# Kernel optimization log

Hardware: AMD Instinct MI355X
Metric: run time of the kernel (lower is better)

## Reference

```python
import jax, jax.numpy as jnp
import numpy as np

D_MODEL = 1024
N_HEADS = 16
N_GROUPS = 4
D_HEAD = D_MODEL // N_HEADS  # 64
HPG = N_HEADS // N_GROUPS    # heads per KV group = 4
B, T = 2, 2048


def _rope(x):
    # x: [B, H, T, D]; interleaved even/odd rotary, matching the torch module
    t, d = x.shape[2], x.shape[3]
    pos = jnp.arange(t, dtype=jnp.float32)[:, None]                      # [T,1]
    freq = jnp.exp(-(jnp.arange(0, d, 2, dtype=jnp.float32) / d)
                   * jnp.log(jnp.float32(10000.0)))                      # [D/2]
    angle = pos * freq                                                   # [T, D/2]
    cos, sin = jnp.cos(angle), jnp.sin(angle)
    xe, xo = x[..., ::2], x[..., 1::2]
    re = xe * cos - xo * sin
    ro = xe * sin + xo * cos
    return jnp.stack([re, ro], axis=-1).reshape(x.shape)


def setup_inputs() -> dict:
    key = jax.random.key(0)
    ks = jax.random.split(key, 10)
    s = 0.02
    return {
        "x":  jax.random.normal(ks[0], (B, T, D_MODEL), dtype=jnp.float32),
        "Wq": jax.random.normal(ks[1], (D_MODEL, D_MODEL), dtype=jnp.float32) * s,
        "bq": jax.random.normal(ks[2], (D_MODEL,), dtype=jnp.float32) * s,
        "Wk": jax.random.normal(ks[3], (D_MODEL, N_GROUPS * D_HEAD), dtype=jnp.float32) * s,
        "bk": jax.random.normal(ks[4], (N_GROUPS * D_HEAD,), dtype=jnp.float32) * s,
        "Wv": jax.random.normal(ks[5], (D_MODEL, N_GROUPS * D_HEAD), dtype=jnp.float32) * s,
        "bv": jax.random.normal(ks[6], (N_GROUPS * D_HEAD,), dtype=jnp.float32) * s,
        "Wo": jax.random.normal(ks[7], (D_MODEL, D_MODEL), dtype=jnp.float32) * s,
        "bo": jax.random.normal(ks[8], (D_MODEL,), dtype=jnp.float32) * s,
    }


def reference(x, Wq, bq, Wk, bk, Wv, bv, Wo, bo):
    b, t, _ = x.shape
    q = (x @ Wq + bq).reshape(b, t, N_HEADS, D_HEAD).transpose(0, 2, 1, 3)    # [B,H,T,D]
    k = (x @ Wk + bk).reshape(b, t, N_GROUPS, D_HEAD).transpose(0, 2, 1, 3)   # [B,G,T,D]
    v = (x @ Wv + bv).reshape(b, t, N_GROUPS, D_HEAD).transpose(0, 2, 1, 3)
    # GQA broadcast: idx = arange(n_heads) // heads_per_group  ==  repeat each group HPG times
    k = jnp.repeat(k, HPG, axis=1)                                            # [B,H,T,D]
    v = jnp.repeat(v, HPG, axis=1)
    q = _rope(q)
    k = _rope(k)
    scale = jnp.float32(np.sqrt(D_HEAD))
    scores = jnp.einsum('bhtd,bhsd->bhts', q, k) / scale                      # [B,H,T,T]
    causal = jnp.tril(jnp.ones((t, t), dtype=bool))
    scores = jnp.where(causal, scores, -jnp.inf)
    probs = jax.nn.softmax(scores, axis=-1)
    # dropout(p=0.05) is identity in eval mode
    attn = jnp.einsum('bhts,bhsd->bhtd', probs, v)
    out = attn.transpose(0, 2, 1, 3).reshape(b, t, N_HEADS * D_HEAD)
    return out @ Wo + bo
```

## Files before the change

kernel.cpp:

```cpp
#include <hip/hip_runtime.h>
#include <stdint.h>

typedef unsigned short u16;
typedef __attribute__((ext_vector_type(4))) float f32x4;
typedef __attribute__((ext_vector_type(8))) short bf16x8;
typedef __attribute__((ext_vector_type(4))) short bf16x4;

#define T_SEQ 2048
#define DM 1024
#define NH 16
#define NG 4
#define DH 64
#define QSCALE 0.18033688011112042f

__device__ __forceinline__ u16 f2bf(float f) {
    union { float f; uint32_t u; } v; v.f = f;
    uint32_t r = (v.u + 0x7FFFu + ((v.u >> 16) & 1u)) >> 16;
    return (u16)r;
}
__device__ __forceinline__ float bf2f(u16 u) {
    union { uint32_t u; float f; } v; v.u = ((uint32_t)u) << 16;
    return v.f;
}
__device__ __forceinline__ float fexp2(float x) {
#if __has_builtin(__builtin_amdgcn_exp2f)
    return __builtin_amdgcn_exp2f(x);
#else
    return exp2f(x);
#endif
}
__device__ __forceinline__ uint32_t cvtpk_bf16(float a, float b) {
    uint32_t r;
    asm("v_cvt_pk_bf16_f32 %0, %1, %2" : "=v"(r) : "v"(a), "v"(b));
    return r;
}

#if __has_builtin(__builtin_amdgcn_mfma_f32_16x16x16_bf16)
__device__ __forceinline__ f32x4 mfma16(bf16x4 a, bf16x4 b, f32x4 c) {
    return __builtin_amdgcn_mfma_f32_16x16x16_bf16(a, b, c, 0, 0, 0);
}
#elif __has_builtin(__builtin_amdgcn_mfma_f32_16x16x16bf16_1k)
__device__ __forceinline__ f32x4 mfma16(bf16x4 a, bf16x4 b, f32x4 c) {
    return __builtin_amdgcn_mfma_f32_16x16x16bf16_1k(a, b, c, 0, 0, 0);
}
#else
__device__ __forceinline__ f32x4 mfma16(bf16x4 a, bf16x4 b, f32x4 c) {
    asm("v_mfma_f32_16x16x16_bf16 %0, %1, %2, %0" : "+v"(c) : "v"(a), "v"(b));
    return c;
}
#endif

__device__ __forceinline__ void async16(const void* g, void* l) {
    __builtin_amdgcn_global_load_lds(
        (const __attribute__((address_space(1))) void*)g,
        (__attribute__((address_space(3))) void*)l,
        16, 0, 0);
}

__global__ __launch_bounds__(256) void k_prep(
    const float* __restrict__ x, u16* __restrict__ xb,
    const float* __restrict__ Wq, const float* __restrict__ Wk,
    const float* __restrict__ Wv, const float* __restrict__ Wo,
    u16* __restrict__ wqkvt, u16* __restrict__ wot,
    const float* __restrict__ bq, const float* __restrict__ bk,
    const float* __restrict__ bv, float* __restrict__ bqkv,
    float2* __restrict__ tbl) {
    int blk = blockIdx.x;
    int tid = threadIdx.x;
    if (blk < 2048) {
        int i = blk * 256 + tid;
        const float4* p = (const float4*)x + (size_t)i * 2;
        float4 a = p[0], b = p[1];
        bf16x8 v;
        v[0] = (short)f2bf(a.x); v[1] = (short)f2bf(a.y);
        v[2] = (short)f2bf(a.z); v[3] = (short)f2bf(a.w);
        v[4] = (short)f2bf(b.x); v[5] = (short)f2bf(b.y);
        v[6] = (short)f2bf(b.z); v[7] = (short)f2bf(b.w);
        ((bf16x8*)xb)[i] = v;
        return;
    }
    int t = blk - 2048;
    if (t >= 2560) {
        int u = t - 2560;
        if (u < 6) {
            int i = u * 256 + tid;
            if (i < 1536) {
                float v;
                if (i < 1024) v = bq[i];
                else if (i < 1280) v = bk[i - 1024];
                else v = bv[i - 1280];
                bqkv[i] = v;
            }
        } else {
            int idx = (u - 6) * 256 + tid;
            int tt = idx >> 5, i = idx & 31;
            float freq = exp2f(-(float)i * (13.287712379549449f / 32.0f));
            float ang = (float)tt * freq;
            tbl[idx] = make_float2(cosf(ang), sinf(ang));
        }
        return;
    }
    const float* src; u16* dst; int N;
    if (t < 1024)      { src = Wq; dst = wqkvt;                      N = 1024; }
    else if (t < 1280) { t -= 1024; src = Wk; dst = wqkvt + (size_t)1024 * 1024; N = 256; }
    else if (t < 1536) { t -= 1280; src = Wv; dst = wqkvt + (size_t)1280 * 1024; N = 256; }
    else               { t -= 1536; src = Wo; dst = wot;             N = 1024; }
    int ntiles = N >> 5;
    int n0 = (t % ntiles) * 32, k0 = (t / ntiles) * 32;
    __shared__ float tile[32][33];
    int tx = tid & 31, ty = tid >> 5;
#pragma unroll
    for (int q = 0; q < 4; q++)
        tile[ty + q * 8][tx] = src[(size_t)(k0 + ty + q * 8) * N + n0 + tx];
    __syncthreads();
#pragma unroll
    for (int q = 0; q < 4; q++)
        dst[(size_t)(n0 + ty + q * 8) * 1024 + k0 + tx] = f2bf(tile[tx][ty + q * 8]);
}

template <int EPI>
__global__ __launch_bounds__(256) void k_gemm(
    const u16* __restrict__ A, const u16* __restrict__ Bt,
    const float* __restrict__ bias, float* __restrict__ C,
    const float2* __restrict__ tbl, u16* __restrict__ Qo,
    u16* __restrict__ Ko, u16* __restrict__ Vto, int N, int K) {
    __shared__ __align__(16) u16 As[2][64 * 64];
    __shared__ __align__(16) u16 Bs[2][128 * 64];
    int tid = threadIdx.x;
    int lane = tid & 63, wid = tid >> 6;
    int wr = wid >> 1, wc = wid & 1;
    int l15 = lane & 15, lhi = lane >> 4;
    int row0 = blockIdx.y * 64, col0 = blockIdx.x * 128;
    f32x4 acc[2][4] = {};

    const u16* ga[2];
    const u16* gb[4];
#pragma unroll
    for (int i = 0; i < 2; i++) {
        int c = i * 256 + tid, r = c >> 3, sch = (c & 7) ^ (r & 7);
        ga[i] = A + (size_t)(row0 + r) * K + sch * 8;
    }
#pragma unroll
    for (int i = 0; i < 4; i++) {
        int c = i * 256 + tid, r = c >> 3, sch = (c & 7) ^ (r & 7);
        gb[i] = Bt + (size_t)(col0 + r) * K + sch * 8;
    }

#pragma unroll
    for (int i = 0; i < 2; i++) async16(ga[i], &As[0][(i * 256 + tid) * 8]);
#pragma unroll
    for (int i = 0; i < 4; i++) async16(gb[i], &Bs[0][(i * 256 + tid) * 8]);
    __syncthreads();

    int nk = K >> 6;
    for (int kt = 0; kt < nk; kt++) {
        int cur = kt & 1;
        if (kt + 1 < nk) {
            int nx = cur ^ 1, ko = (kt + 1) << 6;
#pragma unroll
            for (int i = 0; i < 2; i++) async16(ga[i] + ko, &As[nx][(i * 256 + tid) * 8]);
#pragma unroll
            for (int i = 0; i < 4; i++) async16(gb[i] + ko, &Bs[nx][(i * 256 + tid) * 8]);
        }
        const u16* Ac = As[cur];
        const u16* Bc = Bs[cur];
#pragma unroll
        for (int ks = 0; ks < 2; ks++) {
            bf16x8 af[2], bfr[4];
#pragma unroll
            for (int m = 0; m < 2; m++) {
                int r = wr * 32 + m * 16 + l15;
                int kb = (ks * 64 + lhi * 16) ^ ((r & 7) << 4);
                af[m] = *(const bf16x8*)((const char*)Ac + r * 128 + kb);
            }
#pragma unroll
            for (int n = 0; n < 4; n++) {
                int r = wc * 64 + n * 16 + l15;
                int kb = (ks * 64 + lhi * 16) ^ ((r & 7) << 4);
                bfr[n] = *(const bf16x8*)((const char*)Bc + r * 128 + kb);
            }
#pragma unroll
            for (int m = 0; m < 2; m++)
#pragma unroll
                for (int n = 0; n < 4; n++)
                    acc[m][n] = __builtin_amdgcn_mfma_f32_16x16x32_bf16(
                        af[m], bfr[n], acc[m][n], 0, 0, 0);
        }
        __syncthreads();
    }

    if (EPI == 0) {
#pragma unroll
        for (int n = 0; n < 4; n++) {
            int col = col0 + wc * 64 + n * 16 + l15;
            float bv = bias[col];
#pragma unroll
            for (int m = 0; m < 2; m++) {
                int row = row0 + wr * 32 + m * 16 + lhi * 4;
#pragma unroll
                for (int i = 0; i < 4; i++)
                    C[(size_t)(row + i) * N + col] = acc[m][n][i] + bv;
            }
        }
    } else {
        int type = (col0 >= 1280) ? 2 : (col0 >= 1024 ? 1 : 0);
        int rbase = row0 + wr * 32;
#pragma unroll
        for (int n = 0; n < 4; n++) {
            int col = col0 + wc * 64 + n * 16 + l15;
            float bv = bias[col];
            if (type == 2) {
                int cc = col - 1280;
                int g = cc >> 6, d = cc & 63;
#pragma unroll
                for (int m = 0; m < 2; m++)
#pragma unroll
                    for (int i = 0; i < 4; i++) {
                        int rowg = rbase + m * 16 + lhi * 4 + i;
                        int t = rowg & (T_SEQ - 1), b = rowg >> 11;
                        int sp = t ^ ((d & 1) << 2);
                        Vto[(((size_t)(b * NG + g)) * DH + d) * T_SEQ + sp] =
                            f2bf(acc[m][n][i] + bv);
                    }
            } else {
                float ssgn = (col & 1) ? 1.f : -1.f;
                int ip = (col & 63) >> 1;
#pragma unroll
                for (int m = 0; m < 2; m++)
#pragma unroll
                    for (int i = 0; i < 4; i++) {
                        int rowg = rbase + m * 16 + lhi * 4 + i;
                        int t = rowg & (T_SEQ - 1), b = rowg >> 11;
                        float v = acc[m][n][i] + bv;
                        float other = __shfl_xor(v, 1);
                        float2 cs = tbl[t * 32 + ip];
                        float out = v * cs.x + other * cs.y * ssgn;
                        if (type == 0) {
                            int h = col >> 6, d = col & 63;
                            Qo[(((size_t)(b * NH + h)) * T_SEQ + t) * DH + d] =
                                f2bf(out * QSCALE);
                        } else {
                            int cc = col - 1024;
                            int g = cc >> 6, d = cc & 63;
                            Ko[(((size_t)(b * NG + g)) * T_SEQ + t) * DH + d] = f2bf(out);
                        }
                    }
            }
        }
    }
}

__global__ __launch_bounds__(256) void k_attn(
    const u16* __restrict__ Q, const u16* __restrict__ K,
    const u16* __restrict__ Vt, u16* __restrict__ Aout) {
    int i0 = blockIdx.x;
    int u = i0 >> 5;
    int qt = (u < 16) ? (31 - u) : (u - 16);
    int bh = i0 & 31;
    int b = bh >> 4, h = bh & 15, g = h >> 2;
    int tid = threadIdx.x;
    int lane = tid & 63, wid = tid >> 6;
    int l15 = lane & 15, lhi = lane >> 4;

    const u16* Kp = K + ((size_t)(b * NG + g)) * T_SEQ * DH;
    const u16* Vp = Vt + ((size_t)(b * NG + g)) * DH * T_SEQ;

    __shared__ __align__(16) u16 Ks[2][64 * 64];
    __shared__ __align__(16) u16 Vs[3][64 * 64];

    const u16* Qp = Q + ((size_t)bh * T_SEQ + qt * 64) * DH;
    bf16x8 qf[2];
#pragma unroll
    for (int ks = 0; ks < 2; ks++)
        qf[ks] = *(const bf16x8*)(Qp + (size_t)(wid * 16 + l15) * DH + ks * 32 + lhi * 8);

    f32x4 of[4] = {};
    float l_i = 0.f;

    int nt = qt + 1;
    int swz = (l15 & 7) << 4;

    int c0 = tid, c1 = tid + 256;
    int rk0 = c0 >> 3, rk1 = c1 >> 3;
    int sk0 = (c0 & 7) ^ (rk0 & 7);
    int sk1 = (c1 & 7) ^ (rk1 & 7);
    int sv0 = (c0 & 7) ^ ((rk0 >> 1) & 7);
    int sv1 = (c1 & 7) ^ ((rk1 >> 1) & 7);
    const u16* kg0 = Kp + rk0 * DH + sk0 * 8;
    const u16* kg1 = Kp + rk1 * DH + sk1 * 8;
    const u16* vg0 = Vp + (size_t)rk0 * T_SEQ + sv0 * 8;
    const u16* vg1 = Vp + (size_t)rk1 * T_SEQ + sv1 * 8;

    async16(kg0, &Ks[0][c0 * 8]);
    async16(kg1, &Ks[0][c1 * 8]);
    async16(vg0, &Vs[0][c0 * 8]);
    async16(vg1, &Vs[0][c1 * 8]);
    __syncthreads();
    if (nt > 1) {
        async16(kg0 + (1 << 12), &Ks[1][c0 * 8]);
        async16(kg1 + (1 << 12), &Ks[1][c1 * 8]);
        async16(vg0 + (1 << 6), &Vs[1][c0 * 8]);
        async16(vg1 + (1 << 6), &Vs[1][c1 * 8]);
    }
    f32x4 sf[4] = {};
    __builtin_amdgcn_s_setprio(1);
#pragma unroll
    for (int ks = 0; ks < 2; ks++)
#pragma unroll
        for (int n = 0; n < 4; n++) {
            int kb = (ks * 64 + lhi * 16) ^ swz;
            bf16x8 kf = *(const bf16x8*)((const char*)Ks[0] + (n * 16 + l15) * 128 + kb);
            sf[n] = __builtin_amdgcn_mfma_f32_16x16x32_bf16(kf, qf[ks], sf[n], 0, 0, 0);
        }
    __builtin_amdgcn_s_setprio(0);
    __syncthreads();

    u16* vread = Vs[0];
    u16* vhold = Vs[1];
    u16* vstage = Vs[2];

#pragma unroll 1
    for (int it = 1; it < nt; it++) {
        if (it + 1 < nt) {
            int ko = (it + 1) << 12, vo = (it + 1) << 6;
            int nx = (it + 1) & 1;
            async16(kg0 + ko, &Ks[nx][c0 * 8]);
            async16(kg1 + ko, &Ks[nx][c1 * 8]);
            async16(vg0 + vo, vstage + c0 * 8);
            async16(vg1 + vo, vstage + c1 * 8);
        }

        bf16x4 pa[4];
#pragma unroll
        for (int n = 0; n < 4; n++) {
            float p0 = fexp2(sf[n][0]);
            float p1 = fexp2(sf[n][1]);
            float p2 = fexp2(sf[n][2]);
            float p3 = fexp2(sf[n][3]);
            l_i += p0 + p1 + p2 + p3;
            union { uint32_t uu[2]; bf16x4 v; } pu;
            pu.uu[0] = cvtpk_bf16(p0, p1);
            pu.uu[1] = cvtpk_bf16(p2, p3);
            pa[n] = pu.v;
        }

        const u16* Kc = Ks[it & 1];
        __builtin_amdgcn_s_setprio(1);
#pragma unroll
        for (int ks = 0; ks < 2; ks++)
#pragma unroll
            for (int n = 0; n < 4; n++) {
                int kb = (ks * 64 + lhi * 16) ^ swz;
                bf16x8 kf = *(const bf16x8*)((const char*)Kc + (n * 16 + l15) * 128 + kb);
                f32x4 z = (ks == 0) ? f32x4{0.f, 0.f, 0.f, 0.f} : sf[n];
                sf[n] = __builtin_amdgcn_mfma_f32_16x16x32_bf16(kf, qf[ks], z, 0, 0, 0);
            }

#pragma unroll
        for (int nd = 0; nd < 4; nd++) {
            int rowb = (nd * 16 + l15) * 128;
#pragma unroll
            for (int n = 0; n < 4; n++) {
                int kb = ((4 * n + lhi) ^ l15) << 3;
                bf16x4 vf = *(const bf16x4*)((const char*)vread + rowb + kb);
                of[nd] = mfma16(pa[n], vf, of[nd]);
            }
        }
        __builtin_amdgcn_s_setprio(0);

        u16* tmp = vread; vread = vhold; vhold = vstage; vstage = tmp;
        __syncthreads();
    }

    {
        int qrow = qt * 64 + wid * 16 + l15;
        int sb = (nt - 1) * 64 + lhi * 4;
#pragma unroll
        for (int n = 0; n < 4; n++)
#pragma unroll
            for (int i = 0; i < 4; i++)
                if (sb + n * 16 + i > qrow) sf[n][i] = -3.0e38f;
        bf16x4 pa[4];
#pragma unroll
        for (int n = 0; n < 4; n++) {
            float p0 = fexp2(sf[n][0]);
            float p1 = fexp2(sf[n][1]);
            float p2 = fexp2(sf[n][2]);
            float p3 = fexp2(sf[n][3]);
            l_i += p0 + p1 + p2 + p3;
            union { uint32_t uu[2]; bf16x4 v; } pu;
            pu.uu[0] = cvtpk_bf16(p0, p1);
            pu.uu[1] = cvtpk_bf16(p2, p3);
            pa[n] = pu.v;
        }
        __builtin_amdgcn_s_setprio(1);
#pragma unroll
        for (int nd = 0; nd < 4; nd++) {
            int rowb = (nd * 16 + l15) * 128;
#pragma unroll
            for (int n = 0; n < 4; n++) {
                int kb = ((4 * n + lhi) ^ l15) << 3;
                bf16x4 vf = *(const bf16x4*)((const char*)vread + rowb + kb);
                of[nd] = mfma16(pa[n], vf, of[nd]);
            }
        }
        __builtin_amdgcn_s_setprio(0);
    }

#pragma unroll
    for (int off = 16; off <= 32; off <<= 1)
        l_i += __shfl_xor(l_i, off);
    float lq[4];
#pragma unroll
    for (int i = 0; i < 4; i++)
        lq[i] = __shfl(l_i, lhi * 4 + i);
#pragma unroll
    for (int n = 0; n < 4; n++)
#pragma unroll
        for (int i = 0; i < 4; i++) {
            int trow = qt * 64 + wid * 16 + lhi * 4 + i;
            float v = of[n][i] / lq[i];
            Aout[((size_t)(b * T_SEQ + trow)) * DM + h * 64 + n * 16 + l15] = f2bf(v);
        }
}

extern "C" void kernel_launch(void* const* d_in, const int* in_sizes, int n_in,
                              void* d_out, int out_size, void* d_ws, size_t ws_size,
                              hipStream_t stream) {
    const float* x  = (const float*)d_in[0];
    const float* Wq = (const float*)d_in[1];
    const float* bq = (const float*)d_in[2];
    const float* Wk = (const float*)d_in[3];
    const float* bk = (const float*)d_in[4];
    const float* Wv = (const float*)d_in[5];
    const float* bv = (const float*)d_in[6];
    const float* Wo = (const float*)d_in[7];
    const float* bo = (const float*)d_in[8];

    char* ws = (char*)d_ws;
    size_t o = 0;
    u16*   xb    = (u16*)(ws + o);  o += (size_t)4096 * 1024 * 2;
    u16*   wqkvt = (u16*)(ws + o);  o += (size_t)1536 * 1024 * 2;
    u16*   wot   = (u16*)(ws + o);  o += (size_t)1024 * 1024 * 2;
    float* bqkv  = (float*)(ws + o); o += 1536 * 4;
    o = (o + 255) & ~(size_t)255;
    u16*   Qb    = (u16*)(ws + o);  o += (size_t)2 * NH * T_SEQ * DH * 2;
    u16*   Kb    = (u16*)(ws + o);  o += (size_t)2 * NG * T_SEQ * DH * 2;
    u16*   Vtb   = (u16*)(ws + o);  o += (size_t)2 * NG * DH * T_SEQ * 2;
    u16*   attnb = (u16*)(ws + o);  o += (size_t)4096 * 1024 * 2;
    float2* tbl  = (float2*)(ws + o); o += (size_t)2048 * 32 * 8;

    k_prep<<<4870, 256, 0, stream>>>(x, xb, Wq, Wk, Wv, Wo, wqkvt, wot, bq, bk, bv, bqkv, tbl);
    k_gemm<1><<<dim3(12, 64), 256, 0, stream>>>(xb, wqkvt, bqkv, nullptr, tbl, Qb, Kb, Vtb, 1536, 1024);
    k_attn<<<1024, 256, 0, stream>>>(Qb, Kb, Vtb, attnb);
    k_gemm<0><<<dim3(8, 64), 256, 0, stream>>>(attnb, wot, bo, (float*)d_out, nullptr, nullptr, nullptr, nullptr, 1024, 1024);
}
```

Measured before the change: 87.37 us.

## Process two 64-row query tiles per attention block to reuse K/V tiles

Each attention workgroup now handles 128 query rows (two 64-row sub-tiles) instead of 64, so every K/V tile staged into shared memory feeds twice as many MFMAs. The grid is halved to 512 blocks and the causal masking is split across the two sub-tiles' diagonal steps. The aim is to cut global-to-LDS traffic and barrier overhead per unit of work. In exchange, register pressure roughly doubles for scores and accumulators, and there are fewer blocks to balance the causal workload across CUs.

```diff
diff --git a/kernel.cpp b/kernel.cpp
--- a/kernel.cpp
+++ b/kernel.cpp
@@ -255,7 +255,7 @@
     const u16* __restrict__ Vt, u16* __restrict__ Aout) {
     int i0 = blockIdx.x;
     int u = i0 >> 5;
-    int qt = (u < 16) ? (31 - u) : (u - 16);
+    int qt = (u < 8) ? (15 - u) : (u - 8);
     int bh = i0 & 31;
     int b = bh >> 4, h = bh & 15, g = h >> 2;
     int tid = threadIdx.x;
@@ -268,16 +268,19 @@
     __shared__ __align__(16) u16 Ks[2][64 * 64];
     __shared__ __align__(16) u16 Vs[3][64 * 64];
 
-    const u16* Qp = Q + ((size_t)bh * T_SEQ + qt * 64) * DH;
-    bf16x8 qf[2];
-#pragma unroll
-    for (int ks = 0; ks < 2; ks++)
-        qf[ks] = *(const bf16x8*)(Qp + (size_t)(wid * 16 + l15) * DH + ks * 32 + lhi * 8);
-
-    f32x4 of[4] = {};
-    float l_i = 0.f;
-
-    int nt = qt + 1;
+    const u16* Qp = Q + ((size_t)bh * T_SEQ + qt * 128) * DH;
+    bf16x8 qf[2][2];
+#pragma unroll
+    for (int qq = 0; qq < 2; qq++)
+#pragma unroll
+        for (int ks = 0; ks < 2; ks++)
+            qf[qq][ks] = *(const bf16x8*)(Qp + (size_t)(qq * 64 + wid * 16 + l15) * DH +
+                                          ks * 32 + lhi * 8);
+
+    f32x4 of[2][4] = {};
+    float l0 = 0.f, l1 = 0.f;
+
+    int nt = 2 * qt + 2;
     int swz = (l15 & 7) << 4;
 
     int c0 = tid, c1 = tid + 256;
@@ -296,13 +299,13 @@
     async16(vg0, &Vs[0][c0 * 8]);
     async16(vg1, &Vs[0][c1 * 8]);
     __syncthreads();
-    if (nt > 1) {
+    {
         async16(kg0 + (1 << 12), &Ks[1][c0 * 8]);
         async16(kg1 + (1 << 12), &Ks[1][c1 * 8]);
         async16(vg0 + (1 << 6), &Vs[1][c0 * 8]);
         async16(vg1 + (1 << 6), &Vs[1][c1 * 8]);
     }
-    f32x4 sf[4] = {};
+    f32x4 sf[2][4] = {};
     __builtin_amdgcn_s_setprio(1);
 #pragma unroll
     for (int ks = 0; ks < 2; ks++)
@@ -310,7 +313,8 @@
         for (int n = 0; n < 4; n++) {
             int kb = (ks * 64 + lhi * 16) ^ swz;
             bf16x8 kf = *(const bf16x8*)((const char*)Ks[0] + (n * 16 + l15) * 128 + kb);
-            sf[n] = __builtin_amdgcn_mfma_f32_16x16x32_bf16(kf, qf[ks], sf[n], 0, 0, 0);
+            sf[0][n] = __builtin_amdgcn_mfma_f32_16x16x32_bf16(kf, qf[0][ks], sf[0][n], 0, 0, 0);
+            sf[1][n] = __builtin_amdgcn_mfma_f32_16x16x32_bf16(kf, qf[1][ks], sf[1][n], 0, 0, 0);
         }
     __builtin_amdgcn_s_setprio(0);
     __syncthreads();
@@ -330,18 +334,33 @@
             async16(vg1 + vo, vstage + c1 * 8);
         }
 
-        bf16x4 pa[4];
+        if (it == nt - 1) {
+            int qrow = qt * 128 + wid * 16 + l15;
+            int sb = (nt - 2) * 64 + lhi * 4;
+#pragma unroll
+            for (int n = 0; n < 4; n++)
+#pragma unroll
+                for (int i = 0; i < 4; i++)
+                    if (sb + n * 16 + i > qrow) sf[0][n][i] = -3.0e38f;
+        }
+
+        bf16x4 pa[2][4];
 #pragma unroll
         for (int n = 0; n < 4; n++) {
-            float p0 = fexp2(sf[n][0]);
-            float p1 = fexp2(sf[n][1]);
-            float p2 = fexp2(sf[n][2]);
-            float p3 = fexp2(sf[n][3]);
-            l_i += p0 + p1 + p2 + p3;
+            float a0 = fexp2(sf[0][n][0]), a1 = fexp2(sf[0][n][1]);
+            float a2 = fexp2(sf[0][n][2]), a3 = fexp2(sf[0][n][3]);
+            l0 += a0 + a1 + a2 + a3;
             union { uint32_t uu[2]; bf16x4 v; } pu;
-            pu.uu[0] = cvtpk_bf16(p0, p1);
-            pu.uu[1] = cvtpk_bf16(p2, p3);
-            pa[n] = pu.v;
+            pu.uu[0] = cvtpk_bf16(a0, a1);
+            pu.uu[1] = cvtpk_bf16(a2, a3);
+            pa[0][n] = pu.v;
+            float b0 = fexp2(sf[1][n][0]), b1 = fexp2(sf[1][n][1]);
+            float b2 = fexp2(sf[1][n][2]), b3 = fexp2(sf[1][n][3]);
+            l1 += b0 + b1 + b2 + b3;
+            union { uint32_t uu[2]; bf16x4 v; } pv;
+            pv.uu[0] = cvtpk_bf16(b0, b1);
+            pv.uu[1] = cvtpk_bf16(b2, b3);
+            pa[1][n] = pv.v;
         }
 
         const u16* Kc = Ks[it & 1];
@@ -352,8 +371,10 @@
             for (int n = 0; n < 4; n++) {
                 int kb = (ks * 64 + lhi * 16) ^ swz;
                 bf16x8 kf = *(const bf16x8*)((const char*)Kc + (n * 16 + l15) * 128 + kb);
-                f32x4 z = (ks == 0) ? f32x4{0.f, 0.f, 0.f, 0.f} : sf[n];
-                sf[n] = __builtin_amdgcn_mfma_f32_16x16x32_bf16(kf, qf[ks], z, 0, 0, 0);
+                f32x4 z0 = (ks == 0) ? f32x4{0.f, 0.f, 0.f, 0.f} : sf[0][n];
+                f32x4 z1 = (ks == 0) ? f32x4{0.f, 0.f, 0.f, 0.f} : sf[1][n];
+                sf[0][n] = __builtin_amdgcn_mfma_f32_16x16x32_bf16(kf, qf[0][ks], z0, 0, 0, 0);
+                sf[1][n] = __builtin_amdgcn_mfma_f32_16x16x32_bf16(kf, qf[1][ks], z1, 0, 0, 0);
             }
 
 #pragma unroll
@@ -363,7 +384,8 @@
             for (int n = 0; n < 4; n++) {
                 int kb = ((4 * n + lhi) ^ l15) << 3;
                 bf16x4 vf = *(const bf16x4*)((const char*)vread + rowb + kb);
-                of[nd] = mfma16(pa[n], vf, of[nd]);
+                of[0][nd] = mfma16(pa[0][n], vf, of[0][nd]);
+                of[1][nd] = mfma16(pa[1][n], vf, of[1][nd]);
             }
         }
         __builtin_amdgcn_s_setprio(0);
@@ -373,25 +395,28 @@
     }
 
     {
-        int qrow = qt * 64 + wid * 16 + l15;
+#pragma unroll
+        for (int n = 0; n < 4; n++)
+#pragma unroll
+            for (int i = 0; i < 4; i++)
+                sf[0][n][i] = -3.0e38f;
+        int qrow = qt * 128 + 64 + wid * 16 + l15;
         int sb = (nt - 1) * 64 + lhi * 4;
 #pragma unroll
         for (int n = 0; n < 4; n++)
 #pragma unroll
             for (int i = 0; i < 4; i++)
-                if (sb + n * 16 + i > qrow) sf[n][i] = -3.0e38f;
-        bf16x4 pa[4];
+                if (sb + n * 16 + i > qrow) sf[1][n][i] = -3.0e38f;
+        bf16x4 pa[2][4];
 #pragma unroll
         for (int n = 0; n < 4; n++) {
-            float p0 = fexp2(sf[n][0]);
-            float p1 = fexp2(sf[n][1]);
-            float p2 = fexp2(sf[n][2]);
-            float p3 = fexp2(sf[n][3]);
-            l_i += p0 + p1 + p2 + p3;
-            union { uint32_t uu[2]; bf16x4 v; } pu;
-            pu.uu[0] = cvtpk_bf16(p0, p1);
-            pu.uu[1] = cvtpk_bf16(p2, p3);
-            pa[n] = pu.v;
+            float b0 = fexp2(sf[1][n][0]), b1 = fexp2(sf[1][n][1]);
+            float b2 = fexp2(sf[1][n][2]), b3 = fexp2(sf[1][n][3]);
+            l1 += b0 + b1 + b2 + b3;
+            union { uint32_t uu[2]; bf16x4 v; } pv;
+            pv.uu[0] = cvtpk_bf16(b0, b1);
+            pv.uu[1] = cvtpk_bf16(b2, b3);
+            pa[1][n] = pv.v;
         }
         __builtin_amdgcn_s_setprio(1);
 #pragma unroll
@@ -401,27 +426,34 @@
             for (int n = 0; n < 4; n++) {
                 int kb = ((4 * n + lhi) ^ l15) << 3;
                 bf16x4 vf = *(const bf16x4*)((const char*)vread + rowb + kb);
-                of[nd] = mfma16(pa[n], vf, of[nd]);
+                of[1][nd] = mfma16(pa[1][n], vf, of[1][nd]);
             }
         }
         __builtin_amdgcn_s_setprio(0);
-    }
-
-#pragma unroll
-    for (int off = 16; off <= 32; off <<= 1)
-        l_i += __shfl_xor(l_i, off);
-    float lq[4];
-#pragma unroll
-    for (int i = 0; i < 4; i++)
-        lq[i] = __shfl(l_i, lhi * 4 + i);
-#pragma unroll
-    for (int n = 0; n < 4; n++)
-#pragma unroll
-        for (int i = 0; i < 4; i++) {
-            int trow = qt * 64 + wid * 16 + lhi * 4 + i;
-            float v = of[n][i] / lq[i];
-            Aout[((size_t)(b * T_SEQ + trow)) * DM + h * 64 + n * 16 + l15] = f2bf(v);
-        }
+        (void)pa[0];
+    }
+
+#pragma unroll
+    for (int off = 16; off <= 32; off <<= 1) {
+        l0 += __shfl_xor(l0, off);
+        l1 += __shfl_xor(l1, off);
+    }
+#pragma unroll
+    for (int qq = 0; qq < 2; qq++) {
+        float lsrc = qq ? l1 : l0;
+        float lq[4];
+#pragma unroll
+        for (int i = 0; i < 4; i++)
+            lq[i] = __shfl(lsrc, lhi * 4 + i);
+#pragma unroll
+        for (int n = 0; n < 4; n++)
+#pragma unroll
+            for (int i = 0; i < 4; i++) {
+                int trow = qt * 128 + qq * 64 + wid * 16 + lhi * 4 + i;
+                float v = of[qq][n][i] / lq[i];
+                Aout[((size_t)(b * T_SEQ + trow)) * DM + h * 64 + n * 16 + l15] = f2bf(v);
+            }
+    }
 }
 
 extern "C" void kernel_launch(void* const* d_in, const int* in_sizes, int n_in,
@@ -452,6 +484,6 @@
 
     k_prep<<<4870, 256, 0, stream>>>(x, xb, Wq, Wk, Wv, Wo, wqkvt, wot, bq, bk, bv, bqkv, tbl);
     k_gemm<1><<<dim3(12, 64), 256, 0, stream>>>(xb, wqkvt, bqkv, nullptr, tbl, Qb, Kb, Vtb, 1536, 1024);
-    k_attn<<<1024, 256, 0, stream>>>(Qb, Kb, Vtb, attnb);
+    k_attn<<<512, 256, 0, stream>>>(Qb, Kb, Vtb, attnb);
     k_gemm<0><<<dim3(8, 64), 256, 0, stream>>>(attnb, wot, bo, (float*)d_out, nullptr, nullptr, nullptr, nullptr, 1024, 1024);
 }
```

New measurement: 89.57 us. 2.5% more time.

## Split attention work 2x2 across waves over query and key dimensions

Applied to the files above, without the earlier changes.

Each wave previously owned 16 query rows and the full 64-key tile. Now the waves form a 2x2 grid: each handles 32 query rows and half of the 64 keys, so each K and V fragment read from LDS feeds two MFMAs instead of one. Partial outputs and row sums from the two key-halves are combined at the end through shared memory, which adds an extra barrier and some LDS traffic. The goal is less LDS read pressure per MFMA in the inner loop.

```diff
diff --git a/kernel.cpp b/kernel.cpp
--- a/kernel.cpp
+++ b/kernel.cpp
@@ -260,6 +260,7 @@
     int b = bh >> 4, h = bh & 15, g = h >> 2;
     int tid = threadIdx.x;
     int lane = tid & 63, wid = tid >> 6;
+    int wq = wid & 1, ws = wid >> 1;
     int l15 = lane & 15, lhi = lane >> 4;
 
     const u16* Kp = K + ((size_t)(b * NG + g)) * T_SEQ * DH;
@@ -269,16 +270,21 @@
     __shared__ __align__(16) u16 Vs[3][64 * 64];
 
     const u16* Qp = Q + ((size_t)bh * T_SEQ + qt * 64) * DH;
-    bf16x8 qf[2];
-#pragma unroll
-    for (int ks = 0; ks < 2; ks++)
-        qf[ks] = *(const bf16x8*)(Qp + (size_t)(wid * 16 + l15) * DH + ks * 32 + lhi * 8);
-
-    f32x4 of[4] = {};
-    float l_i = 0.f;
+    bf16x8 qf[2][2];
+#pragma unroll
+    for (int jq = 0; jq < 2; jq++)
+#pragma unroll
+        for (int ks = 0; ks < 2; ks++)
+            qf[jq][ks] = *(const bf16x8*)(Qp + (size_t)(wq * 32 + jq * 16 + l15) * DH +
+                                          ks * 32 + lhi * 8);
+
+    f32x4 of[2][4] = {};
+    float l2[2] = {0.f, 0.f};
 
     int nt = qt + 1;
     int swz = (l15 & 7) << 4;
+    int srow = ws * 32;
+    int vchunkbase = ws * 8;
 
     int c0 = tid, c1 = tid + 256;
     int rk0 = c0 >> 3, rk1 = c1 >> 3;
@@ -302,15 +308,17 @@
         async16(vg0 + (1 << 6), &Vs[1][c0 * 8]);
         async16(vg1 + (1 << 6), &Vs[1][c1 * 8]);
     }
-    f32x4 sf[4] = {};
+    f32x4 sf[2][2] = {};
     __builtin_amdgcn_s_setprio(1);
 #pragma unroll
     for (int ks = 0; ks < 2; ks++)
 #pragma unroll
-        for (int n = 0; n < 4; n++) {
+        for (int sblk = 0; sblk < 2; sblk++) {
             int kb = (ks * 64 + lhi * 16) ^ swz;
-            bf16x8 kf = *(const bf16x8*)((const char*)Ks[0] + (n * 16 + l15) * 128 + kb);
-            sf[n] = __builtin_amdgcn_mfma_f32_16x16x32_bf16(kf, qf[ks], sf[n], 0, 0, 0);
+            bf16x8 kf = *(const bf16x8*)((const char*)Ks[0] +
+                                         (srow + sblk * 16 + l15) * 128 + kb);
+            sf[sblk][0] = __builtin_amdgcn_mfma_f32_16x16x32_bf16(kf, qf[0][ks], sf[sblk][0], 0, 0, 0);
+            sf[sblk][1] = __builtin_amdgcn_mfma_f32_16x16x32_bf16(kf, qf[1][ks], sf[sblk][1], 0, 0, 0);
         }
     __builtin_amdgcn_s_setprio(0);
     __syncthreads();
@@ -330,42 +338,47 @@
             async16(vg1 + vo, vstage + c1 * 8);
         }
 
-        bf16x4 pa[4];
-#pragma unroll
-        for (int n = 0; n < 4; n++) {
-            float p0 = fexp2(sf[n][0]);
-            float p1 = fexp2(sf[n][1]);
-            float p2 = fexp2(sf[n][2]);
-            float p3 = fexp2(sf[n][3]);
-            l_i += p0 + p1 + p2 + p3;
-            union { uint32_t uu[2]; bf16x4 v; } pu;
-            pu.uu[0] = cvtpk_bf16(p0, p1);
-            pu.uu[1] = cvtpk_bf16(p2, p3);
-            pa[n] = pu.v;
-        }
+        bf16x4 pa[2][2];
+#pragma unroll
+        for (int sblk = 0; sblk < 2; sblk++)
+#pragma unroll
+            for (int jq = 0; jq < 2; jq++) {
+                float p0 = fexp2(sf[sblk][jq][0]);
+                float p1 = fexp2(sf[sblk][jq][1]);
+                float p2 = fexp2(sf[sblk][jq][2]);
+                float p3 = fexp2(sf[sblk][jq][3]);
+                l2[jq] += p0 + p1 + p2 + p3;
+                union { uint32_t uu[2]; bf16x4 v; } pu;
+                pu.uu[0] = cvtpk_bf16(p0, p1);
+                pu.uu[1] = cvtpk_bf16(p2, p3);
+                pa[sblk][jq] = pu.v;
+            }
 
         const u16* Kc = Ks[it & 1];
         __builtin_amdgcn_s_setprio(1);
 #pragma unroll
         for (int ks = 0; ks < 2; ks++)
 #pragma unroll
-            for (int n = 0; n < 4; n++) {
+            for (int sblk = 0; sblk < 2; sblk++) {
                 int kb = (ks * 64 + lhi * 16) ^ swz;
-                bf16x8 kf = *(const bf16x8*)((const char*)Kc + (n * 16 + l15) * 128 + kb);
-                f32x4 z = (ks == 0) ? f32x4{0.f, 0.f, 0.f, 0.f} : sf[n];
-                sf[n] = __builtin_amdgcn_mfma_f32_16x16x32_bf16(kf, qf[ks], z, 0, 0, 0);
-            }
-
-#pragma unroll
-        for (int nd = 0; nd < 4; nd++) {
-            int rowb = (nd * 16 + l15) * 128;
-#pragma unroll
-            for (int n = 0; n < 4; n++) {
-                int kb = ((4 * n + lhi) ^ l15) << 3;
+                bf16x8 kf = *(const bf16x8*)((const char*)Kc +
+                                             (srow + sblk * 16 + l15) * 128 + kb);
+                f32x4 z0 = (ks == 0) ? f32x4{0.f, 0.f, 0.f, 0.f} : sf[sblk][0];
+                f32x4 z1 = (ks == 0) ? f32x4{0.f, 0.f, 0.f, 0.f} : sf[sblk][1];
+                sf[sblk][0] = __builtin_amdgcn_mfma_f32_16x16x32_bf16(kf, qf[0][ks], z0, 0, 0, 0);
+                sf[sblk][1] = __builtin_amdgcn_mfma_f32_16x16x32_bf16(kf, qf[1][ks], z1, 0, 0, 0);
+            }
+
+#pragma unroll
+        for (int sblk = 0; sblk < 2; sblk++)
+#pragma unroll
+            for (int nd = 0; nd < 4; nd++) {
+                int rowb = (nd * 16 + l15) * 128;
+                int kb = ((vchunkbase + sblk * 4 + lhi) ^ l15) << 3;
                 bf16x4 vf = *(const bf16x4*)((const char*)vread + rowb + kb);
-                of[nd] = mfma16(pa[n], vf, of[nd]);
-            }
-        }
+                of[0][nd] = mfma16(pa[sblk][0], vf, of[0][nd]);
+                of[1][nd] = mfma16(pa[sblk][1], vf, of[1][nd]);
+            }
         __builtin_amdgcn_s_setprio(0);
 
         u16* tmp = vread; vread = vhold; vhold = vstage; vstage = tmp;
@@ -373,55 +386,91 @@
     }
 
     {
-        int qrow = qt * 64 + wid * 16 + l15;
-        int sb = (nt - 1) * 64 + lhi * 4;
-#pragma unroll
-        for (int n = 0; n < 4; n++)
+        int sb = (nt - 1) * 64 + srow + lhi * 4;
+        int qb = qt * 64 + wq * 32 + l15;
+#pragma unroll
+        for (int sblk = 0; sblk < 2; sblk++)
+#pragma unroll
+            for (int jq = 0; jq < 2; jq++)
+#pragma unroll
+                for (int i = 0; i < 4; i++)
+                    if (sb + sblk * 16 + i > qb + jq * 16) sf[sblk][jq][i] = -3.0e38f;
+        bf16x4 pa[2][2];
+#pragma unroll
+        for (int sblk = 0; sblk < 2; sblk++)
+#pragma unroll
+            for (int jq = 0; jq < 2; jq++) {
+                float p0 = fexp2(sf[sblk][jq][0]);
+                float p1 = fexp2(sf[sblk][jq][1]);
+                float p2 = fexp2(sf[sblk][jq][2]);
+                float p3 = fexp2(sf[sblk][jq][3]);
+                l2[jq] += p0 + p1 + p2 + p3;
+                union { uint32_t uu[2]; bf16x4 v; } pu;
+                pu.uu[0] = cvtpk_bf16(p0, p1);
+                pu.uu[1] = cvtpk_bf16(p2, p3);
+                pa[sblk][jq] = pu.v;
+            }
+        __builtin_amdgcn_s_setprio(1);
+#pragma unroll
+        for (int sblk = 0; sblk < 2; sblk++)
+#pragma unroll
+            for (int nd = 0; nd < 4; nd++) {
+                int rowb = (nd * 16 + l15) * 128;
+                int kb = ((vchunkbase + sblk * 4 + lhi) ^ l15) << 3;
+                bf16x4 vf = *(const bf16x4*)((const char*)vread + rowb + kb);
+                of[0][nd] = mfma16(pa[sblk][0], vf, of[0][nd]);
+                of[1][nd] = mfma16(pa[sblk][1], vf, of[1][nd]);
+            }
+        __builtin_amdgcn_s_setprio(0);
+    }
+
+#pragma unroll
+    for (int off = 16; off <= 32; off <<= 1) {
+        l2[0] += __shfl_xor(l2[0], off);
+        l2[1] += __shfl_xor(l2[1], off);
+    }
+
+    __syncthreads();
+    float* Osh = (float*)Vs;
+    float* Lsh = (float*)Ks;
+    if (ws == 1) {
+#pragma unroll
+        for (int jq = 0; jq < 2; jq++)
+#pragma unroll
+            for (int nd = 0; nd < 4; nd++)
+#pragma unroll
+                for (int i = 0; i < 4; i++)
+                    Osh[wq * 2176 + (jq * 16 + lhi * 4 + i) * 68 + nd * 16 + l15] =
+                        of[jq][nd][i];
+        if (lhi == 0) {
+            Lsh[wq * 32 + l15] = l2[0];
+            Lsh[wq * 32 + 16 + l15] = l2[1];
+        }
+    }
+    __syncthreads();
+    if (ws == 0) {
+        float lt[2];
+        lt[0] = l2[0] + Lsh[wq * 32 + l15];
+        lt[1] = l2[1] + Lsh[wq * 32 + 16 + l15];
+        float lq[2][4];
+#pragma unroll
+        for (int jq = 0; jq < 2; jq++)
 #pragma unroll
             for (int i = 0; i < 4; i++)
-                if (sb + n * 16 + i > qrow) sf[n][i] = -3.0e38f;
-        bf16x4 pa[4];
-#pragma unroll
-        for (int n = 0; n < 4; n++) {
-            float p0 = fexp2(sf[n][0]);
-            float p1 = fexp2(sf[n][1]);
-            float p2 = fexp2(sf[n][2]);
-            float p3 = fexp2(sf[n][3]);
-            l_i += p0 + p1 + p2 + p3;
-            union { uint32_t uu[2]; bf16x4 v; } pu;
-            pu.uu[0] = cvtpk_bf16(p0, p1);
-            pu.uu[1] = cvtpk_bf16(p2, p3);
-            pa[n] = pu.v;
-        }
-        __builtin_amdgcn_s_setprio(1);
-#pragma unroll
-        for (int nd = 0; nd < 4; nd++) {
-            int rowb = (nd * 16 + l15) * 128;
-#pragma unroll
-            for (int n = 0; n < 4; n++) {
-                int kb = ((4 * n + lhi) ^ l15) << 3;
-                bf16x4 vf = *(const bf16x4*)((const char*)vread + rowb + kb);
-                of[nd] = mfma16(pa[n], vf, of[nd]);
-            }
-        }
-        __builtin_amdgcn_s_setprio(0);
-    }
-
-#pragma unroll
-    for (int off = 16; off <= 32; off <<= 1)
-        l_i += __shfl_xor(l_i, off);
-    float lq[4];
-#pragma unroll
-    for (int i = 0; i < 4; i++)
-        lq[i] = __shfl(l_i, lhi * 4 + i);
-#pragma unroll
-    for (int n = 0; n < 4; n++)
-#pragma unroll
-        for (int i = 0; i < 4; i++) {
-            int trow = qt * 64 + wid * 16 + lhi * 4 + i;
-            float v = of[n][i] / lq[i];
-            Aout[((size_t)(b * T_SEQ + trow)) * DM + h * 64 + n * 16 + l15] = f2bf(v);
-        }
+                lq[jq][i] = __shfl(lt[jq], lhi * 4 + i);
+#pragma unroll
+        for (int jq = 0; jq < 2; jq++)
+#pragma unroll
+            for (int nd = 0; nd < 4; nd++)
+#pragma unroll
+                for (int i = 0; i < 4; i++) {
+                    float v = of[jq][nd][i] +
+                              Osh[wq * 2176 + (jq * 16 + lhi * 4 + i) * 68 + nd * 16 + l15];
+                    int trow = qt * 64 + wq * 32 + jq * 16 + lhi * 4 + i;
+                    Aout[((size_t)(b * T_SEQ + trow)) * DM + h * 64 + nd * 16 + l15] =
+                        f2bf(v / lq[jq][i]);
+                }
+    }
 }
 
 extern "C" void kernel_launch(void* const* d_in, const int* in_sizes, int n_in,
```

Result: no change. 86.25 us (median of 2 runs) (-1.3%).
